# Kernel tuning notes

Hardware: AMD Instinct MI355X
Metric: run time of the kernel (lower is better)

Reference implementation:

```python
import jax, jax.numpy as jnp
import numpy as np

N, C, E = 50000, 128, 600000


def setup_inputs() -> dict:
    key = jax.random.key(0)
    ks = jax.random.split(key, 10)
    s = 1.0 / np.sqrt(C)
    x = jax.random.normal(ks[0], (N, C), jnp.float32)
    edge_index = jax.random.randint(ks[1], (2, E), 0, N)
    edge_weight = jax.random.uniform(ks[2], (E,), jnp.float32)
    # learned params
    p_score = jax.random.normal(ks[3], (C,), jnp.float32) * s      # TopKPooling projection
    W0 = jax.random.normal(ks[4], (C, C), jnp.float32) * s         # initial GCN weight
    w_ih = jax.random.normal(ks[5], (3 * C, C), jnp.float32) * s   # GRU input weights (r,z,n)
    w_hh = jax.random.normal(ks[6], (3 * C, C), jnp.float32) * s   # GRU hidden weights
    b_ih = jnp.zeros((3 * C,), jnp.float32)
    b_hh = jnp.zeros((3 * C,), jnp.float32)
    w_lin = jax.random.normal(ks[7], (1, C), jnp.float32) * s      # head Linear(C,1)
    b_lin = jnp.zeros((1,), jnp.float32)
    return dict(x=x, edge_index=edge_index, edge_weight=edge_weight,
                p_score=p_score, W0=W0, w_ih=w_ih, w_hh=w_hh,
                b_ih=b_ih, b_hh=b_hh, w_lin=w_lin, b_lin=b_lin)


def _evolve_gcnh(x, edge_index, edge_weight, p_score, W0, w_ih, w_hh, b_ih, b_hh):
    n, c = x.shape
    # --- TopKPooling: score = tanh((x.p)/||p||), keep top k=C nodes, scale by score
    score = jnp.tanh((x @ p_score) / jnp.linalg.norm(p_score))
    vals, perm = jax.lax.top_k(score, c)           # tanh monotone -> same perm as raw score
    x_tilde = x[perm] * vals[:, None]              # [C, C]
    # --- GRU single step: batch = C rows of the weight matrix, hidden = W0
    gi = x_tilde @ w_ih.T + b_ih                   # [C, 3C]
    gh = W0 @ w_hh.T + b_hh                        # [C, 3C]
    i_r, i_z, i_n = jnp.split(gi, 3, axis=1)
    h_r, h_z, h_n = jnp.split(gh, 3, axis=1)
    r = jax.nn.sigmoid(i_r + h_r)
    z = jax.nn.sigmoid(i_z + h_z)
    ng = jnp.tanh(i_n + r * h_n)
    W = (1.0 - z) * ng + z * W0                    # evolved GCN weight [C, C]
    # --- GCNConv with fixed W: gcn_norm with self loops, then scatter-sum
    loops = jnp.arange(n)
    row = jnp.concatenate([edge_index[0], loops])  # source
    col = jnp.concatenate([edge_index[1], loops])  # target
    w = jnp.concatenate([edge_weight, jnp.ones((n,), edge_weight.dtype)])
    deg = jax.ops.segment_sum(w, col, num_segments=n)
    dis = jnp.where(deg > 0, jax.lax.rsqrt(jnp.where(deg > 0, deg, 1.0)), 0.0)
    norm = dis[row] * w * dis[col]                 # [E+N]
    xw = x @ W                                     # [N, C]
    out = jax.ops.segment_sum(norm[:, None] * xw[row], col, num_segments=n)
    return out


def reference(x, edge_index, edge_weight, p_score, W0, w_ih, w_hh, b_ih, b_hh, w_lin, b_lin):
    h = _evolve_gcnh(x, edge_index, edge_weight, p_score, W0, w_ih, w_hh, b_ih, b_hh)
    h = jax.nn.relu(h)
    return h @ w_lin.T + b_lin                     # [N, 1]
```

## Files before the change

kernel.cpp:

```cpp
#include <hip/hip_runtime.h>
#include <stdint.h>

#define C 128
#define RSTRIDE 64

typedef __attribute__((ext_vector_type(8))) short short8;
typedef __attribute__((ext_vector_type(4))) float f32x4;

__device__ __forceinline__ unsigned f32_orderable(float f) {
  unsigned u = __float_as_uint(f);
  return (u & 0x80000000u) ? ~u : (u | 0x80000000u);
}
__device__ __forceinline__ unsigned short f32_to_bf16_rn(float f) {
  unsigned u = __float_as_uint(f);
  unsigned rounding = 0x7FFFu + ((u >> 16) & 1u);
  return (unsigned short)((u + rounding) >> 16);
}
__device__ __forceinline__ float bf16_to_f32(unsigned short h) {
  return __uint_as_float(((unsigned)h) << 16);
}

__global__ __launch_bounds__(256) void k_score(const float* __restrict__ x,
                                               const float* __restrict__ p,
                                               float* __restrict__ score,
                                               unsigned* __restrict__ hist, int N) {
  int l = threadIdx.x & 63;
  int n = blockIdx.x * 4 + (threadIdx.x >> 6);
  if (n >= N) return;
  float2 xv = ((const float2*)(x + (size_t)n * C))[l];
  float2 pv = ((const float2*)p)[l];
  float s = xv.x * pv.x + xv.y * pv.y;
  for (int o = 32; o > 0; o >>= 1) s += __shfl_down(s, o, 64);
  if (l == 0) {
    score[n] = s;
    atomicAdd(&hist[f32_orderable(s) >> 16], 1u);
  }
}

__global__ void k_thresh(const unsigned* __restrict__ hist, unsigned* __restrict__ misc_u) {
  __shared__ unsigned csum[1024];
  __shared__ int tcs;
  int t = threadIdx.x;
  unsigned s = 0;
  const unsigned* hb = hist + t * 64;
  for (int b = 0; b < 64; ++b) s += hb[b];
  csum[t] = s;
  __syncthreads();
  for (int off = 1; off < 1024; off <<= 1) {
    unsigned v = (t + off < 1024) ? csum[t + off] : 0u;
    __syncthreads();
    csum[t] += v;
    __syncthreads();
  }
  unsigned St  = csum[t];
  unsigned St1 = (t < 1023) ? csum[t + 1] : 0u;
  if (St >= 128u && St1 < 128u) tcs = t;
  __syncthreads();
  if (t == 0) {
    int tc = tcs;
    unsigned cum = (tc < 1023) ? csum[tc + 1] : 0u;
    unsigned T = (unsigned)(tc * 64);
    for (int b = tc * 64 + 63; b >= tc * 64; --b) {
      cum += hist[b];
      if (cum >= 128u) { T = (unsigned)b; break; }
    }
    misc_u[1] = T;
  }
}

__global__ __launch_bounds__(256) void k_collect(const float* __restrict__ score,
                                                 unsigned* __restrict__ misc_u,
                                                 uint64_t* __restrict__ cand, int N) {
  int n = blockIdx.x * 256 + threadIdx.x;
  if (n >= N) return;
  unsigned T = misc_u[1];
  unsigned u = f32_orderable(score[n]);
  if ((u >> 16) >= T) {
    unsigned pos = atomicAdd(&misc_u[0], 1u);
    if (pos < 1024u) cand[pos] = ((uint64_t)u << 32) | (unsigned)(~n);
  }
}

__global__ void k_select(const unsigned* __restrict__ misc_u,
                         const float* __restrict__ p,
                         const uint64_t* __restrict__ cand,
                         int* __restrict__ perm, float* __restrict__ vals) {
  __shared__ uint64_t keys[1024];
  __shared__ float s_inv;
  int t = threadIdx.x;
  if (t < 64) {
    float2 v = ((const float2*)p)[t];
    float s = v.x * v.x + v.y * v.y;
    for (int o = 32; o > 0; o >>= 1) s += __shfl_down(s, o, 64);
    if (t == 0) s_inv = 1.0f / sqrtf(s);
  }
  unsigned M = misc_u[0];
  if (M > 1024u) M = 1024u;
  keys[t] = (t < (int)M) ? cand[t] : 0ull;
  __syncthreads();
  for (int size = 2; size <= 1024; size <<= 1) {
    for (int stride = size >> 1; stride > 0; stride >>= 1) {
      int pr = t ^ stride;
      if (pr > t) {
        uint64_t a = keys[t], b = keys[pr];
        bool desc = ((t & size) == 0);
        if (desc ? (a < b) : (a > b)) { keys[t] = b; keys[pr] = a; }
      }
      __syncthreads();
    }
  }
  if (t < C) {
    uint64_t key = keys[t];
    unsigned n = ~(unsigned)(key & 0xFFFFFFFFull);
    unsigned u = (unsigned)(key >> 32);
    unsigned bbits = (u & 0x80000000u) ? (u & 0x7FFFFFFFu) : ~u;
    float s = __uint_as_float(bbits);
    perm[t] = (int)n;
    vals[t] = tanhf(s * s_inv);
  }
}

__global__ __launch_bounds__(128) void k_gru(const float* __restrict__ x,
                                             const int* __restrict__ perm,
                                             const float* __restrict__ vals,
                                             const float* __restrict__ W0,
                                             const float* __restrict__ w_ih,
                                             const float* __restrict__ w_hh,
                                             const float* __restrict__ b_ih,
                                             const float* __restrict__ b_hh,
                                             float* __restrict__ W) {
  __shared__ float xt[C], h0[C];
  int i = blockIdx.x, j = threadIdx.x;
  xt[j] = x[(size_t)perm[i] * C + j] * vals[i];
  h0[j] = W0[i * C + j];
  __syncthreads();
  float ir = b_ih[j], iz = b_ih[C + j], in_ = b_ih[2 * C + j];
  float hr = b_hh[j], hz = b_hh[C + j], hn  = b_hh[2 * C + j];
  const float4* wr = (const float4*)(w_ih + (size_t)j * C);
  const float4* wz = (const float4*)(w_ih + (size_t)(C + j) * C);
  const float4* wn = (const float4*)(w_ih + (size_t)(2 * C + j) * C);
  const float4* vr = (const float4*)(w_hh + (size_t)j * C);
  const float4* vz = (const float4*)(w_hh + (size_t)(C + j) * C);
  const float4* vn = (const float4*)(w_hh + (size_t)(2 * C + j) * C);
  const float4* xt4 = (const float4*)xt;
  const float4* h04 = (const float4*)h0;
  for (int k = 0; k < C / 4; ++k) {
    float4 xv = xt4[k], hv = h04[k], a;
    a = wr[k]; ir  += xv.x * a.x + xv.y * a.y + xv.z * a.z + xv.w * a.w;
    a = wz[k]; iz  += xv.x * a.x + xv.y * a.y + xv.z * a.z + xv.w * a.w;
    a = wn[k]; in_ += xv.x * a.x + xv.y * a.y + xv.z * a.z + xv.w * a.w;
    a = vr[k]; hr  += hv.x * a.x + hv.y * a.y + hv.z * a.z + hv.w * a.w;
    a = vz[k]; hz  += hv.x * a.x + hv.y * a.y + hv.z * a.z + hv.w * a.w;
    a = vn[k]; hn  += hv.x * a.x + hv.y * a.y + hv.z * a.z + hv.w * a.w;
  }
  float r  = 1.0f / (1.0f + expf(-(ir + hr)));
  float z  = 1.0f / (1.0f + expf(-(iz + hz)));
  float ng = tanhf(in_ + r * hn);
  W[i * C + j] = (1.0f - z) * ng + z * h0[j];
}

__global__ __launch_bounds__(256) void k_wsplit(const float* __restrict__ W,
                                                unsigned short* __restrict__ Bhi,
                                                unsigned short* __restrict__ Blo) {
  int gtid = blockIdx.x * 256 + threadIdx.x;
  int tile = gtid >> 6;
  int l = gtid & 63;
  int ct = tile >> 2, kt = tile & 3;
  int j = ct * 16 + (l & 15);
  int kbase = kt * 32 + (l >> 4) * 8;
  size_t o = (size_t)(tile * 64 + l) * 8;
#pragma unroll
  for (int e = 0; e < 8; ++e) {
    float w = W[(size_t)(kbase + e) * C + j];
    unsigned short hi = f32_to_bf16_rn(w);
    float rem = w - bf16_to_f32(hi);
    Bhi[o + e] = hi;
    Blo[o + e] = f32_to_bf16_rn(rem);
  }
}

__global__ __launch_bounds__(256) void k_xw(const float* __restrict__ x,
                                            const unsigned short* __restrict__ Bhi,
                                            const unsigned short* __restrict__ Blo,
                                            unsigned short* __restrict__ xwh, int N) {
  int wid = threadIdx.x >> 6;
  int l = threadIdx.x & 63;
  int rt = blockIdx.x * 4 + wid;
  int r0 = rt * 16;
  if (r0 >= N) return;
  int row16 = l & 15;
  int kgrp = l >> 4;

  short8 ahi[4], alo[4];
#pragma unroll
  for (int kt = 0; kt < 4; ++kt) {
    int r = r0 + row16;
    if (r >= N) r = N - 1;
    const float* xp = x + (size_t)r * C + kt * 32 + kgrp * 8;
    float4 a0 = *(const float4*)xp;
    float4 a1 = *(const float4*)(xp + 4);
    float v[8] = {a0.x, a0.y, a0.z, a0.w, a1.x, a1.y, a1.z, a1.w};
#pragma unroll
    for (int e = 0; e < 8; ++e) {
      unsigned short hi = f32_to_bf16_rn(v[e]);
      float rem = v[e] - bf16_to_f32(hi);
      ahi[kt][e] = (short)hi;
      alo[kt][e] = (short)f32_to_bf16_rn(rem);
    }
  }

  f32x4 acc[8];
#pragma unroll
  for (int ct = 0; ct < 8; ++ct) acc[ct] = (f32x4){0.f, 0.f, 0.f, 0.f};

#pragma unroll
  for (int ct = 0; ct < 8; ++ct) {
#pragma unroll
    for (int kt = 0; kt < 4; ++kt) {
      const short8 bhi = *(const short8*)(Bhi + (size_t)((ct * 4 + kt) * 64 + l) * 8);
      const short8 blo = *(const short8*)(Blo + (size_t)((ct * 4 + kt) * 64 + l) * 8);
      acc[ct] = __builtin_amdgcn_mfma_f32_16x16x32_bf16(ahi[kt], bhi, acc[ct], 0, 0, 0);
      acc[ct] = __builtin_amdgcn_mfma_f32_16x16x32_bf16(alo[kt], bhi, acc[ct], 0, 0, 0);
      acc[ct] = __builtin_amdgcn_mfma_f32_16x16x32_bf16(ahi[kt], blo, acc[ct], 0, 0, 0);
      acc[ct] = __builtin_amdgcn_mfma_f32_16x16x32_bf16(alo[kt], blo, acc[ct], 0, 0, 0);
    }
  }

#pragma unroll
  for (int ct = 0; ct < 8; ++ct) {
    int col = ct * 16 + row16;
#pragma unroll
    for (int reg = 0; reg < 4; ++reg) {
      int row = r0 + kgrp * 4 + reg;
      if (row < N) xwh[(size_t)row * C + col] = f32_to_bf16_rn(acc[ct][reg]);
    }
  }
}

__global__ __launch_bounds__(256) void k_fill(const int* __restrict__ ei,
                                              const float* __restrict__ ew,
                                              int* __restrict__ cnt,
                                              unsigned* __restrict__ csr, int E) {
  int e = blockIdx.x * 256 + threadIdx.x;
  if (e >= E) return;
  int src = ei[e];
  int dst = ei[E + e];
  int r = atomicAdd(&cnt[dst], 1);
  if (r > RSTRIDE - 1) r = RSTRIDE - 1;
  unsigned ent = ((unsigned)f32_to_bf16_rn(ew[e]) << 16) | (unsigned)src;
  csr[((size_t)dst << 6) + r] = ent;
}

__global__ __launch_bounds__(256) void k_rowdeg(const unsigned* __restrict__ csr,
                                                const int* __restrict__ cnt,
                                                float* __restrict__ dis, int N) {
  int tid = threadIdx.x;
  int n = blockIdx.x * 32 + (tid >> 3);
  if (n >= N) return;
  int l = tid & 7;
  int c = cnt[n];
  if (c > RSTRIDE) c = RSTRIDE;
  const unsigned* row = csr + ((size_t)n << 6);
  float s = 0.0f;
  for (int i = l; i < c; i += 8) s += bf16_to_f32((unsigned short)(row[i] >> 16));
  for (int o = 4; o > 0; o >>= 1) s += __shfl_down(s, o, 8);
  if (l == 0) dis[n] = rsqrtf(1.0f + s);
}

__device__ __forceinline__ float4 bf16x4_to_f32(uint2 pk) {
  float4 r;
  r.x = __uint_as_float(pk.x << 16);
  r.y = __uint_as_float(pk.x & 0xFFFF0000u);
  r.z = __uint_as_float(pk.y << 16);
  r.w = __uint_as_float(pk.y & 0xFFFF0000u);
  return r;
}
__global__ __launch_bounds__(256) void k_gather_final(const unsigned* __restrict__ csr,
                                                      const int* __restrict__ cnt,
                                                      const unsigned short* __restrict__ xwh,
                                                      const float* __restrict__ dis,
                                                      const float* __restrict__ w_lin,
                                                      const float* __restrict__ b_lin,
                                                      float* __restrict__ out, int N) {
  int tid = threadIdx.x;
  int n = blockIdx.x * 8 + (tid >> 5);
  if (n >= N) return;
  int l = tid & 31;
  const unsigned* row = csr + ((size_t)n << 6);
  int c = cnt[n];
  if (c > RSTRIDE) c = RSTRIDE;
  float4 acc = make_float4(0.f, 0.f, 0.f, 0.f);
  int i = 0;
  for (; i + 7 < c; i += 8) {
    unsigned n0 = row[i],   n1 = row[i+1], n2 = row[i+2], n3 = row[i+3];
    unsigned n4 = row[i+4], n5 = row[i+5], n6 = row[i+6], n7 = row[i+7];
    int s0 = n0 & 0xFFFF, s1 = n1 & 0xFFFF, s2 = n2 & 0xFFFF, s3 = n3 & 0xFFFF;
    int s4 = n4 & 0xFFFF, s5 = n5 & 0xFFFF, s6 = n6 & 0xFFFF, s7 = n7 & 0xFFFF;
    float w0 = bf16_to_f32((unsigned short)(n0 >> 16)) * dis[s0];
    float w1 = bf16_to_f32((unsigned short)(n1 >> 16)) * dis[s1];
    float w2 = bf16_to_f32((unsigned short)(n2 >> 16)) * dis[s2];
    float w3 = bf16_to_f32((unsigned short)(n3 >> 16)) * dis[s3];
    float w4 = bf16_to_f32((unsigned short)(n4 >> 16)) * dis[s4];
    float w5 = bf16_to_f32((unsigned short)(n5 >> 16)) * dis[s5];
    float w6 = bf16_to_f32((unsigned short)(n6 >> 16)) * dis[s6];
    float w7 = bf16_to_f32((unsigned short)(n7 >> 16)) * dis[s7];
    uint2 p0 = ((const uint2*)(xwh + (size_t)s0 * C))[l];
    uint2 p1 = ((const uint2*)(xwh + (size_t)s1 * C))[l];
    uint2 p2 = ((const uint2*)(xwh + (size_t)s2 * C))[l];
    uint2 p3 = ((const uint2*)(xwh + (size_t)s3 * C))[l];
    uint2 p4 = ((const uint2*)(xwh + (size_t)s4 * C))[l];
    uint2 p5 = ((const uint2*)(xwh + (size_t)s5 * C))[l];
    uint2 p6 = ((const uint2*)(xwh + (size_t)s6 * C))[l];
    uint2 p7 = ((const uint2*)(xwh + (size_t)s7 * C))[l];
    float4 v0 = bf16x4_to_f32(p0), v1 = bf16x4_to_f32(p1);
    float4 v2 = bf16x4_to_f32(p2), v3 = bf16x4_to_f32(p3);
    float4 v4 = bf16x4_to_f32(p4), v5 = bf16x4_to_f32(p5);
    float4 v6 = bf16x4_to_f32(p6), v7 = bf16x4_to_f32(p7);
    acc.x += w0*v0.x + w1*v1.x + w2*v2.x + w3*v3.x + w4*v4.x + w5*v5.x + w6*v6.x + w7*v7.x;
    acc.y += w0*v0.y + w1*v1.y + w2*v2.y + w3*v3.y + w4*v4.y + w5*v5.y + w6*v6.y + w7*v7.y;
    acc.z += w0*v0.z + w1*v1.z + w2*v2.z + w3*v3.z + w4*v4.z + w5*v5.z + w6*v6.z + w7*v7.z;
    acc.w += w0*v0.w + w1*v1.w + w2*v2.w + w3*v3.w + w4*v4.w + w5*v5.w + w6*v6.w + w7*v7.w;
  }
  for (; i < c; ++i) {
    unsigned n0 = row[i];
    int s0 = n0 & 0xFFFF;
    float w0 = bf16_to_f32((unsigned short)(n0 >> 16)) * dis[s0];
    uint2 p0 = ((const uint2*)(xwh + (size_t)s0 * C))[l];
    float4 v0 = bf16x4_to_f32(p0);
    acc.x += w0 * v0.x;
    acc.y += w0 * v0.y;
    acc.z += w0 * v0.z;
    acc.w += w0 * v0.w;
  }
  float dn = dis[n];
  uint2 ps = ((const uint2*)(xwh + (size_t)n * C))[l];
  float4 xv = bf16x4_to_f32(ps);
  acc.x = fmaf(dn, xv.x, acc.x) * dn;
  acc.y = fmaf(dn, xv.y, acc.y) * dn;
  acc.z = fmaf(dn, xv.z, acc.z) * dn;
  acc.w = fmaf(dn, xv.w, acc.w) * dn;
  float4 wl = ((const float4*)w_lin)[l];
  float psum = fmaxf(acc.x, 0.f) * wl.x + fmaxf(acc.y, 0.f) * wl.y
             + fmaxf(acc.z, 0.f) * wl.z + fmaxf(acc.w, 0.f) * wl.w;
  for (int o = 16; o > 0; o >>= 1) psum += __shfl_down(psum, o, 32);
  if (l == 0) out[n] = psum + b_lin[0];
}

extern "C" void kernel_launch(void* const* d_in, const int* in_sizes, int n_in,
                              void* d_out, int out_size, void* d_ws, size_t ws_size,
                              hipStream_t stream) {
  const float* x     = (const float*)d_in[0];
  const int*   ei    = (const int*)d_in[1];
  const float* ew    = (const float*)d_in[2];
  const float* p     = (const float*)d_in[3];
  const float* W0    = (const float*)d_in[4];
  const float* w_ih  = (const float*)d_in[5];
  const float* w_hh  = (const float*)d_in[6];
  const float* b_ih  = (const float*)d_in[7];
  const float* b_hh  = (const float*)d_in[8];
  const float* w_lin = (const float*)d_in[9];
  const float* b_lin = (const float*)d_in[10];
  int N = in_sizes[0] / C;
  int E = in_sizes[2];
  int NB = (N + 255) / 256;

  char* ws = (char*)d_ws;
  size_t off = 0;
  auto alloc = [&](size_t bytes) -> void* {
    void* q = ws + off;
    off = (off + bytes + 255) & ~(size_t)255;
    return q;
  };
  unsigned short* xwh = (unsigned short*)alloc((size_t)N * C * 2);
  unsigned* csr    = (unsigned*)alloc((size_t)N * RSTRIDE * 4);
  float*    score  = (float*)alloc((size_t)N * 4);
  float*    dis    = (float*)alloc((size_t)N * 4);
  int*      cnt    = (int*)alloc((size_t)N * 4);
  unsigned* hist   = (unsigned*)alloc(65536 * 4);
  uint64_t* cand   = (uint64_t*)alloc(1024 * 8);
  unsigned* misc_u = (unsigned*)alloc(256);
  int*      perm   = (int*)alloc(C * 4);
  float*    vals   = (float*)alloc(C * 4);
  float*    W      = (float*)alloc(C * C * 4);
  unsigned short* Bhi = (unsigned short*)alloc(C * C * 2);
  unsigned short* Blo = (unsigned short*)alloc(C * C * 2);

  hipMemsetAsync(hist, 0, 65536 * 4, stream);
  hipMemsetAsync(misc_u, 0, 256, stream);
  hipMemsetAsync(cnt, 0, (size_t)N * 4, stream);

  k_score<<<(N + 3) / 4, 256, 0, stream>>>(x, p, score, hist, N);
  k_thresh<<<1, 1024, 0, stream>>>(hist, misc_u);
  k_collect<<<NB, 256, 0, stream>>>(score, misc_u, cand, N);
  k_select<<<1, 1024, 0, stream>>>(misc_u, p, cand, perm, vals);
  k_gru<<<C, C, 0, stream>>>(x, perm, vals, W0, w_ih, w_hh, b_ih, b_hh, W);
  k_wsplit<<<8, 256, 0, stream>>>(W, Bhi, Blo);
  {
    int rowtiles = (N + 15) / 16;
    int blocks = (rowtiles + 3) / 4;
    k_xw<<<blocks, 256, 0, stream>>>(x, Bhi, Blo, xwh, N);
  }
  k_fill<<<(E + 255) / 256, 256, 0, stream>>>(ei, ew, cnt, csr, E);
  k_rowdeg<<<(N + 31) / 32, 256, 0, stream>>>(csr, cnt, dis, N);
  k_gather_final<<<(N + 7) / 8, 256, 0, stream>>>(csr, cnt, xwh, dis,
                                                  w_lin, b_lin, (float*)d_out, N);
}
```

Baseline: 258.5 us.

## Fuse score/CSR fill and topk/rowdeg kernels, unroll gather edge loop

After: 259.5 us. About the same (+0.4%).

```diff
diff --git a/kernel.cpp b/kernel.cpp
--- a/kernel.cpp
+++ b/kernel.cpp
@@ -20,103 +20,132 @@
   return __uint_as_float(((unsigned)h) << 16);
 }
 
-__global__ __launch_bounds__(256) void k_score(const float* __restrict__ x,
-                                               const float* __restrict__ p,
-                                               float* __restrict__ score,
-                                               unsigned* __restrict__ hist, int N) {
-  int l = threadIdx.x & 63;
-  int n = blockIdx.x * 4 + (threadIdx.x >> 6);
-  if (n >= N) return;
-  float2 xv = ((const float2*)(x + (size_t)n * C))[l];
-  float2 pv = ((const float2*)p)[l];
-  float s = xv.x * pv.x + xv.y * pv.y;
-  for (int o = 32; o > 0; o >>= 1) s += __shfl_down(s, o, 64);
-  if (l == 0) {
-    score[n] = s;
-    atomicAdd(&hist[f32_orderable(s) >> 16], 1u);
-  }
-}
-
-__global__ void k_thresh(const unsigned* __restrict__ hist, unsigned* __restrict__ misc_u) {
-  __shared__ unsigned csum[1024];
-  __shared__ int tcs;
+__global__ __launch_bounds__(256) void k_score_fill(const float* __restrict__ x,
+                                                    const float* __restrict__ p,
+                                                    float* __restrict__ score,
+                                                    unsigned* __restrict__ hist, int N,
+                                                    const int* __restrict__ ei,
+                                                    const float* __restrict__ ew,
+                                                    int* __restrict__ cnt,
+                                                    unsigned* __restrict__ csr, int E,
+                                                    int SB) {
+  int b = blockIdx.x;
+  if (b < SB) {
+    int l = threadIdx.x & 63;
+    int n = b * 4 + (threadIdx.x >> 6);
+    if (n >= N) return;
+    float2 xv = ((const float2*)(x + (size_t)n * C))[l];
+    float2 pv = ((const float2*)p)[l];
+    float s = xv.x * pv.x + xv.y * pv.y;
+    for (int o = 32; o > 0; o >>= 1) s += __shfl_down(s, o, 64);
+    if (l == 0) {
+      score[n] = s;
+      atomicAdd(&hist[f32_orderable(s) >> 16], 1u);
+    }
+  } else {
+    int e = (b - SB) * 256 + threadIdx.x;
+    if (e >= E) return;
+    int src = ei[e];
+    int dst = ei[E + e];
+    int r = atomicAdd(&cnt[dst], 1);
+    if (r > RSTRIDE - 1) r = RSTRIDE - 1;
+    unsigned ent = ((unsigned)f32_to_bf16_rn(ew[e]) << 16) | (unsigned)src;
+    csr[((size_t)dst << 6) + r] = ent;
+  }
+}
+
+__global__ __launch_bounds__(1024) void k_topk_rowdeg(const unsigned* __restrict__ hist,
+                                                      const float* __restrict__ score,
+                                                      const float* __restrict__ p,
+                                                      int* __restrict__ perm,
+                                                      float* __restrict__ vals, int N,
+                                                      const unsigned* __restrict__ csr,
+                                                      const int* __restrict__ cnt,
+                                                      float* __restrict__ dis) {
   int t = threadIdx.x;
-  unsigned s = 0;
-  const unsigned* hb = hist + t * 64;
-  for (int b = 0; b < 64; ++b) s += hb[b];
-  csum[t] = s;
-  __syncthreads();
-  for (int off = 1; off < 1024; off <<= 1) {
-    unsigned v = (t + off < 1024) ? csum[t + off] : 0u;
-    __syncthreads();
-    csum[t] += v;
-    __syncthreads();
-  }
-  unsigned St  = csum[t];
-  unsigned St1 = (t < 1023) ? csum[t + 1] : 0u;
-  if (St >= 128u && St1 < 128u) tcs = t;
-  __syncthreads();
-  if (t == 0) {
-    int tc = tcs;
-    unsigned cum = (tc < 1023) ? csum[tc + 1] : 0u;
-    unsigned T = (unsigned)(tc * 64);
-    for (int b = tc * 64 + 63; b >= tc * 64; --b) {
-      cum += hist[b];
-      if (cum >= 128u) { T = (unsigned)b; break; }
-    }
-    misc_u[1] = T;
-  }
-}
-
-__global__ __launch_bounds__(256) void k_collect(const float* __restrict__ score,
-                                                 unsigned* __restrict__ misc_u,
-                                                 uint64_t* __restrict__ cand, int N) {
-  int n = blockIdx.x * 256 + threadIdx.x;
-  if (n >= N) return;
-  unsigned T = misc_u[1];
-  unsigned u = f32_orderable(score[n]);
-  if ((u >> 16) >= T) {
-    unsigned pos = atomicAdd(&misc_u[0], 1u);
-    if (pos < 1024u) cand[pos] = ((uint64_t)u << 32) | (unsigned)(~n);
-  }
-}
-
-__global__ void k_select(const unsigned* __restrict__ misc_u,
-                         const float* __restrict__ p,
-                         const uint64_t* __restrict__ cand,
-                         int* __restrict__ perm, float* __restrict__ vals) {
-  __shared__ uint64_t keys[1024];
-  __shared__ float s_inv;
-  int t = threadIdx.x;
-  if (t < 64) {
-    float2 v = ((const float2*)p)[t];
-    float s = v.x * v.x + v.y * v.y;
-    for (int o = 32; o > 0; o >>= 1) s += __shfl_down(s, o, 64);
-    if (t == 0) s_inv = 1.0f / sqrtf(s);
-  }
-  unsigned M = misc_u[0];
-  if (M > 1024u) M = 1024u;
-  keys[t] = (t < (int)M) ? cand[t] : 0ull;
-  __syncthreads();
-  for (int size = 2; size <= 1024; size <<= 1) {
-    for (int stride = size >> 1; stride > 0; stride >>= 1) {
-      int pr = t ^ stride;
-      if (pr > t) {
-        uint64_t a = keys[t], b = keys[pr];
-        bool desc = ((t & size) == 0);
-        if (desc ? (a < b) : (a > b)) { keys[t] = b; keys[pr] = a; }
+  if (blockIdx.x == 0) {
+    __shared__ unsigned csum[1024];
+    __shared__ uint64_t keys[1024];
+    __shared__ int tcs;
+    __shared__ unsigned Ts, cnt_sh;
+    __shared__ float s_inv;
+    if (t < 64) {
+      float2 v = ((const float2*)p)[t];
+      float s = v.x * v.x + v.y * v.y;
+      for (int o = 32; o > 0; o >>= 1) s += __shfl_down(s, o, 64);
+      if (t == 0) s_inv = 1.0f / sqrtf(s);
+    }
+    if (t == 0) cnt_sh = 0;
+    unsigned s = 0;
+    const unsigned* hb = hist + t * 64;
+    for (int b = 0; b < 64; ++b) s += hb[b];
+    csum[t] = s;
+    __syncthreads();
+    for (int off = 1; off < 1024; off <<= 1) {
+      unsigned v = (t + off < 1024) ? csum[t + off] : 0u;
+      __syncthreads();
+      csum[t] += v;
+      __syncthreads();
+    }
+    unsigned St  = csum[t];
+    unsigned St1 = (t < 1023) ? csum[t + 1] : 0u;
+    if (St >= 128u && St1 < 128u) tcs = t;
+    __syncthreads();
+    if (t == 0) {
+      int tc = tcs;
+      unsigned cum = (tc < 1023) ? csum[tc + 1] : 0u;
+      unsigned T = (unsigned)(tc * 64);
+      for (int b = tc * 64 + 63; b >= tc * 64; --b) {
+        cum += hist[b];
+        if (cum >= 128u) { T = (unsigned)b; break; }
       }
-      __syncthreads();
-    }
-  }
-  if (t < C) {
-    uint64_t key = keys[t];
-    unsigned n = ~(unsigned)(key & 0xFFFFFFFFull);
-    unsigned u = (unsigned)(key >> 32);
-    unsigned bbits = (u & 0x80000000u) ? (u & 0x7FFFFFFFu) : ~u;
-    float s = __uint_as_float(bbits);
-    perm[t] = (int)n;
-    vals[t] = tanhf(s * s_inv);
+      Ts = T;
+    }
+    __syncthreads();
+    unsigned T = Ts;
+    for (int k = t; k < N; k += 1024) {
+      unsigned u = f32_orderable(score[k]);
+      if ((u >> 16) >= T) {
+        unsigned pos = atomicAdd(&cnt_sh, 1u);
+        if (pos < 1024u) keys[pos] = ((uint64_t)u << 32) | (unsigned)(~k);
+      }
+    }
+    __syncthreads();
+    unsigned M = cnt_sh;
+    if (M > 1024u) M = 1024u;
+    if (t >= (int)M) keys[t] = 0ull;
+    __syncthreads();
+    for (int size = 2; size <= 1024; size <<= 1) {
+      for (int stride = size >> 1; stride > 0; stride >>= 1) {
+        int pr = t ^ stride;
+        if (pr > t) {
+          uint64_t a = keys[t], b = keys[pr];
+          bool desc = ((t & size) == 0);
+          if (desc ? (a < b) : (a > b)) { keys[t] = b; keys[pr] = a; }
+        }
+        __syncthreads();
+      }
+    }
+    if (t < C) {
+      uint64_t key = keys[t];
+      unsigned n = ~(unsigned)(key & 0xFFFFFFFFull);
+      unsigned u = (unsigned)(key >> 32);
+      unsigned bbits = (u & 0x80000000u) ? (u & 0x7FFFFFFFu) : ~u;
+      float sc = __uint_as_float(bbits);
+      perm[t] = (int)n;
+      vals[t] = tanhf(sc * s_inv);
+    }
+  } else {
+    int n = (blockIdx.x - 1) * 128 + (t >> 3);
+    if (n >= N) return;
+    int l = t & 7;
+    int c = cnt[n];
+    if (c > RSTRIDE) c = RSTRIDE;
+    const unsigned* row = csr + ((size_t)n << 6);
+    float s = 0.0f;
+    for (int i = l; i < c; i += 8) s += bf16_to_f32((unsigned short)(row[i] >> 16));
+    for (int o = 4; o > 0; o >>= 1) s += __shfl_down(s, o, 8);
+    if (l == 0) dis[n] = rsqrtf(1.0f + s);
   }
 }
 
@@ -237,36 +266,6 @@
   }
 }
 
-__global__ __launch_bounds__(256) void k_fill(const int* __restrict__ ei,
-                                              const float* __restrict__ ew,
-                                              int* __restrict__ cnt,
-                                              unsigned* __restrict__ csr, int E) {
-  int e = blockIdx.x * 256 + threadIdx.x;
-  if (e >= E) return;
-  int src = ei[e];
-  int dst = ei[E + e];
-  int r = atomicAdd(&cnt[dst], 1);
-  if (r > RSTRIDE - 1) r = RSTRIDE - 1;
-  unsigned ent = ((unsigned)f32_to_bf16_rn(ew[e]) << 16) | (unsigned)src;
-  csr[((size_t)dst << 6) + r] = ent;
-}
-
-__global__ __launch_bounds__(256) void k_rowdeg(const unsigned* __restrict__ csr,
-                                                const int* __restrict__ cnt,
-                                                float* __restrict__ dis, int N) {
-  int tid = threadIdx.x;
-  int n = blockIdx.x * 32 + (tid >> 3);
-  if (n >= N) return;
-  int l = tid & 7;
-  int c = cnt[n];
-  if (c > RSTRIDE) c = RSTRIDE;
-  const unsigned* row = csr + ((size_t)n << 6);
-  float s = 0.0f;
-  for (int i = l; i < c; i += 8) s += bf16_to_f32((unsigned short)(row[i] >> 16));
-  for (int o = 4; o > 0; o >>= 1) s += __shfl_down(s, o, 8);
-  if (l == 0) dis[n] = rsqrtf(1.0f + s);
-}
-
 __device__ __forceinline__ float4 bf16x4_to_f32(uint2 pk) {
   float4 r;
   r.x = __uint_as_float(pk.x << 16);
@@ -290,47 +289,31 @@
   int c = cnt[n];
   if (c > RSTRIDE) c = RSTRIDE;
   float4 acc = make_float4(0.f, 0.f, 0.f, 0.f);
-  int i = 0;
-  for (; i + 7 < c; i += 8) {
-    unsigned n0 = row[i],   n1 = row[i+1], n2 = row[i+2], n3 = row[i+3];
-    unsigned n4 = row[i+4], n5 = row[i+5], n6 = row[i+6], n7 = row[i+7];
-    int s0 = n0 & 0xFFFF, s1 = n1 & 0xFFFF, s2 = n2 & 0xFFFF, s3 = n3 & 0xFFFF;
-    int s4 = n4 & 0xFFFF, s5 = n5 & 0xFFFF, s6 = n6 & 0xFFFF, s7 = n7 & 0xFFFF;
-    float w0 = bf16_to_f32((unsigned short)(n0 >> 16)) * dis[s0];
-    float w1 = bf16_to_f32((unsigned short)(n1 >> 16)) * dis[s1];
-    float w2 = bf16_to_f32((unsigned short)(n2 >> 16)) * dis[s2];
-    float w3 = bf16_to_f32((unsigned short)(n3 >> 16)) * dis[s3];
-    float w4 = bf16_to_f32((unsigned short)(n4 >> 16)) * dis[s4];
-    float w5 = bf16_to_f32((unsigned short)(n5 >> 16)) * dis[s5];
-    float w6 = bf16_to_f32((unsigned short)(n6 >> 16)) * dis[s6];
-    float w7 = bf16_to_f32((unsigned short)(n7 >> 16)) * dis[s7];
-    uint2 p0 = ((const uint2*)(xwh + (size_t)s0 * C))[l];
-    uint2 p1 = ((const uint2*)(xwh + (size_t)s1 * C))[l];
-    uint2 p2 = ((const uint2*)(xwh + (size_t)s2 * C))[l];
-    uint2 p3 = ((const uint2*)(xwh + (size_t)s3 * C))[l];
-    uint2 p4 = ((const uint2*)(xwh + (size_t)s4 * C))[l];
-    uint2 p5 = ((const uint2*)(xwh + (size_t)s5 * C))[l];
-    uint2 p6 = ((const uint2*)(xwh + (size_t)s6 * C))[l];
-    uint2 p7 = ((const uint2*)(xwh + (size_t)s7 * C))[l];
-    float4 v0 = bf16x4_to_f32(p0), v1 = bf16x4_to_f32(p1);
-    float4 v2 = bf16x4_to_f32(p2), v3 = bf16x4_to_f32(p3);
-    float4 v4 = bf16x4_to_f32(p4), v5 = bf16x4_to_f32(p5);
-    float4 v6 = bf16x4_to_f32(p6), v7 = bf16x4_to_f32(p7);
-    acc.x += w0*v0.x + w1*v1.x + w2*v2.x + w3*v3.x + w4*v4.x + w5*v5.x + w6*v6.x + w7*v7.x;
-    acc.y += w0*v0.y + w1*v1.y + w2*v2.y + w3*v3.y + w4*v4.y + w5*v5.y + w6*v6.y + w7*v7.y;
-    acc.z += w0*v0.z + w1*v1.z + w2*v2.z + w3*v3.z + w4*v4.z + w5*v5.z + w6*v6.z + w7*v7.z;
-    acc.w += w0*v0.w + w1*v1.w + w2*v2.w + w3*v3.w + w4*v4.w + w5*v5.w + w6*v6.w + w7*v7.w;
-  }
-  for (; i < c; ++i) {
-    unsigned n0 = row[i];
-    int s0 = n0 & 0xFFFF;
-    float w0 = bf16_to_f32((unsigned short)(n0 >> 16)) * dis[s0];
-    uint2 p0 = ((const uint2*)(xwh + (size_t)s0 * C))[l];
-    float4 v0 = bf16x4_to_f32(p0);
-    acc.x += w0 * v0.x;
-    acc.y += w0 * v0.y;
-    acc.z += w0 * v0.z;
-    acc.w += w0 * v0.w;
+
+  unsigned ent[16];
+#pragma unroll
+  for (int i = 0; i < 16; ++i) ent[i] = row[i];
+#pragma unroll
+  for (int i = 0; i < 16; ++i) {
+    int si = ent[i] & 0xFFFF;
+    float wi = (i < c) ? bf16_to_f32((unsigned short)(ent[i] >> 16)) * dis[si] : 0.0f;
+    uint2 pk = ((const uint2*)(xwh + (size_t)si * C))[l];
+    float4 v = bf16x4_to_f32(pk);
+    acc.x += wi * v.x;
+    acc.y += wi * v.y;
+    acc.z += wi * v.z;
+    acc.w += wi * v.w;
+  }
+  for (int i = 16; i < c; ++i) {
+    unsigned e0 = row[i];
+    int s0 = e0 & 0xFFFF;
+    float w0 = bf16_to_f32((unsigned short)(e0 >> 16)) * dis[s0];
+    uint2 pk = ((const uint2*)(xwh + (size_t)s0 * C))[l];
+    float4 v = bf16x4_to_f32(pk);
+    acc.x += w0 * v.x;
+    acc.y += w0 * v.y;
+    acc.z += w0 * v.z;
+    acc.w += w0 * v.w;
   }
   float dn = dis[n];
   uint2 ps = ((const uint2*)(xwh + (size_t)n * C))[l];
@@ -362,7 +345,6 @@
   const float* b_lin = (const float*)d_in[10];
   int N = in_sizes[0] / C;
   int E = in_sizes[2];
-  int NB = (N + 255) / 256;
 
   char* ws = (char*)d_ws;
   size_t off = 0;
@@ -375,24 +357,23 @@
   unsigned* csr    = (unsigned*)alloc((size_t)N * RSTRIDE * 4);
   float*    score  = (float*)alloc((size_t)N * 4);
   float*    dis    = (float*)alloc((size_t)N * 4);
+  size_t zstart = off;
+  unsigned* hist   = (unsigned*)alloc(65536 * 4);
   int*      cnt    = (int*)alloc((size_t)N * 4);
-  unsigned* hist   = (unsigned*)alloc(65536 * 4);
-  uint64_t* cand   = (uint64_t*)alloc(1024 * 8);
-  unsigned* misc_u = (unsigned*)alloc(256);
+  size_t zend = off;
   int*      perm   = (int*)alloc(C * 4);
   float*    vals   = (float*)alloc(C * 4);
   float*    W      = (float*)alloc(C * C * 4);
   unsigned short* Bhi = (unsigned short*)alloc(C * C * 2);
   unsigned short* Blo = (unsigned short*)alloc(C * C * 2);
 
-  hipMemsetAsync(hist, 0, 65536 * 4, stream);
-  hipMemsetAsync(misc_u, 0, 256, stream);
-  hipMemsetAsync(cnt, 0, (size_t)N * 4, stream);
-
-  k_score<<<(N + 3) / 4, 256, 0, stream>>>(x, p, score, hist, N);
-  k_thresh<<<1, 1024, 0, stream>>>(hist, misc_u);
-  k_collect<<<NB, 256, 0, stream>>>(score, misc_u, cand, N);
-  k_select<<<1, 1024, 0, stream>>>(misc_u, p, cand, perm, vals);
+  hipMemsetAsync(ws + zstart, 0, zend - zstart, stream);
+
+  int SB = (N + 3) / 4;
+  int FB = (E + 255) / 256;
+  k_score_fill<<<SB + FB, 256, 0, stream>>>(x, p, score, hist, N, ei, ew, cnt, csr, E, SB);
+  int RB = (N + 127) / 128;
+  k_topk_rowdeg<<<1 + RB, 1024, 0, stream>>>(hist, score, p, perm, vals, N, csr, cnt, dis);
   k_gru<<<C, C, 0, stream>>>(x, perm, vals, W0, w_ih, w_hh, b_ih, b_hh, W);
   k_wsplit<<<8, 256, 0, stream>>>(W, Bhi, Blo);
   {
@@ -400,8 +381,6 @@
     int blocks = (rowtiles + 3) / 4;
     k_xw<<<blocks, 256, 0, stream>>>(x, Bhi, Blo, xwh, N);
   }
-  k_fill<<<(E + 255) / 256, 256, 0, stream>>>(ei, ew, cnt, csr, E);
-  k_rowdeg<<<(N + 31) / 32, 256, 0, stream>>>(csr, cnt, dis, N);
   k_gather_final<<<(N + 7) / 8, 256, 0, stream>>>(csr, cnt, xwh, dis,
                                                   w_lin, b_lin, (float*)d_out, N);
 }
```

## Fuse top-k selection stages with row-degree pass and fold W split into GRU

Applied to the files above, without the earlier changes.

New measurement: 267.8 us. +3.6%, slower.

```diff
diff --git a/kernel.cpp b/kernel.cpp
--- a/kernel.cpp
+++ b/kernel.cpp
@@ -18,6 +18,14 @@
 }
 __device__ __forceinline__ float bf16_to_f32(unsigned short h) {
   return __uint_as_float(((unsigned)h) << 16);
+}
+__device__ __forceinline__ float4 bf16x4_to_f32(uint2 pk) {
+  float4 r;
+  r.x = __uint_as_float(pk.x << 16);
+  r.y = __uint_as_float(pk.x & 0xFFFF0000u);
+  r.z = __uint_as_float(pk.y << 16);
+  r.w = __uint_as_float(pk.y & 0xFFFF0000u);
+  return r;
 }
 
 __global__ __launch_bounds__(256) void k_score(const float* __restrict__ x,
@@ -37,86 +45,111 @@
   }
 }
 
-__global__ void k_thresh(const unsigned* __restrict__ hist, unsigned* __restrict__ misc_u) {
-  __shared__ unsigned csum[1024];
-  __shared__ int tcs;
+__global__ __launch_bounds__(256) void k_fill(const int* __restrict__ ei,
+                                              const float* __restrict__ ew,
+                                              int* __restrict__ cnt,
+                                              unsigned* __restrict__ csr, int E) {
+  int e = blockIdx.x * 256 + threadIdx.x;
+  if (e >= E) return;
+  int src = ei[e];
+  int dst = ei[E + e];
+  int r = atomicAdd(&cnt[dst], 1);
+  if (r > RSTRIDE - 1) r = RSTRIDE - 1;
+  unsigned ent = ((unsigned)f32_to_bf16_rn(ew[e]) << 16) | (unsigned)src;
+  csr[((size_t)dst << 6) + r] = ent;
+}
+
+__global__ __launch_bounds__(1024) void k_topk_rowdeg(const unsigned* __restrict__ hist,
+                                                      const float* __restrict__ score,
+                                                      const float* __restrict__ p,
+                                                      int* __restrict__ perm,
+                                                      float* __restrict__ vals, int N,
+                                                      const unsigned* __restrict__ csr,
+                                                      const int* __restrict__ cnt,
+                                                      float* __restrict__ dis) {
   int t = threadIdx.x;
-  unsigned s = 0;
-  const unsigned* hb = hist + t * 64;
-  for (int b = 0; b < 64; ++b) s += hb[b];
-  csum[t] = s;
-  __syncthreads();
-  for (int off = 1; off < 1024; off <<= 1) {
-    unsigned v = (t + off < 1024) ? csum[t + off] : 0u;
-    __syncthreads();
-    csum[t] += v;
-    __syncthreads();
-  }
-  unsigned St  = csum[t];
-  unsigned St1 = (t < 1023) ? csum[t + 1] : 0u;
-  if (St >= 128u && St1 < 128u) tcs = t;
-  __syncthreads();
-  if (t == 0) {
-    int tc = tcs;
-    unsigned cum = (tc < 1023) ? csum[tc + 1] : 0u;
-    unsigned T = (unsigned)(tc * 64);
-    for (int b = tc * 64 + 63; b >= tc * 64; --b) {
-      cum += hist[b];
-      if (cum >= 128u) { T = (unsigned)b; break; }
-    }
-    misc_u[1] = T;
-  }
-}
-
-__global__ __launch_bounds__(256) void k_collect(const float* __restrict__ score,
-                                                 unsigned* __restrict__ misc_u,
-                                                 uint64_t* __restrict__ cand, int N) {
-  int n = blockIdx.x * 256 + threadIdx.x;
-  if (n >= N) return;
-  unsigned T = misc_u[1];
-  unsigned u = f32_orderable(score[n]);
-  if ((u >> 16) >= T) {
-    unsigned pos = atomicAdd(&misc_u[0], 1u);
-    if (pos < 1024u) cand[pos] = ((uint64_t)u << 32) | (unsigned)(~n);
-  }
-}
-
-__global__ void k_select(const unsigned* __restrict__ misc_u,
-                         const float* __restrict__ p,
-                         const uint64_t* __restrict__ cand,
-                         int* __restrict__ perm, float* __restrict__ vals) {
-  __shared__ uint64_t keys[1024];
-  __shared__ float s_inv;
-  int t = threadIdx.x;
-  if (t < 64) {
-    float2 v = ((const float2*)p)[t];
-    float s = v.x * v.x + v.y * v.y;
-    for (int o = 32; o > 0; o >>= 1) s += __shfl_down(s, o, 64);
-    if (t == 0) s_inv = 1.0f / sqrtf(s);
-  }
-  unsigned M = misc_u[0];
-  if (M > 1024u) M = 1024u;
-  keys[t] = (t < (int)M) ? cand[t] : 0ull;
-  __syncthreads();
-  for (int size = 2; size <= 1024; size <<= 1) {
-    for (int stride = size >> 1; stride > 0; stride >>= 1) {
-      int pr = t ^ stride;
-      if (pr > t) {
-        uint64_t a = keys[t], b = keys[pr];
-        bool desc = ((t & size) == 0);
-        if (desc ? (a < b) : (a > b)) { keys[t] = b; keys[pr] = a; }
+  if (blockIdx.x == 0) {
+    __shared__ unsigned csum[1024];
+    __shared__ uint64_t keys[1024];
+    __shared__ int tcs;
+    __shared__ unsigned Ts, cnt_sh;
+    __shared__ float s_inv;
+    if (t < 64) {
+      float2 v = ((const float2*)p)[t];
+      float s = v.x * v.x + v.y * v.y;
+      for (int o = 32; o > 0; o >>= 1) s += __shfl_down(s, o, 64);
+      if (t == 0) s_inv = 1.0f / sqrtf(s);
+    }
+    if (t == 0) cnt_sh = 0;
+    unsigned s = 0;
+    const unsigned* hb = hist + t * 64;
+    for (int b = 0; b < 64; ++b) s += hb[b];
+    csum[t] = s;
+    __syncthreads();
+    for (int off = 1; off < 1024; off <<= 1) {
+      unsigned v = (t + off < 1024) ? csum[t + off] : 0u;
+      __syncthreads();
+      csum[t] += v;
+      __syncthreads();
+    }
+    unsigned St  = csum[t];
+    unsigned St1 = (t < 1023) ? csum[t + 1] : 0u;
+    if (St >= 128u && St1 < 128u) tcs = t;
+    __syncthreads();
+    if (t == 0) {
+      int tc = tcs;
+      unsigned cum = (tc < 1023) ? csum[tc + 1] : 0u;
+      unsigned T = (unsigned)(tc * 64);
+      for (int b = tc * 64 + 63; b >= tc * 64; --b) {
+        cum += hist[b];
+        if (cum >= 128u) { T = (unsigned)b; break; }
       }
-      __syncthreads();
-    }
-  }
-  if (t < C) {
-    uint64_t key = keys[t];
-    unsigned n = ~(unsigned)(key & 0xFFFFFFFFull);
-    unsigned u = (unsigned)(key >> 32);
-    unsigned bbits = (u & 0x80000000u) ? (u & 0x7FFFFFFFu) : ~u;
-    float s = __uint_as_float(bbits);
-    perm[t] = (int)n;
-    vals[t] = tanhf(s * s_inv);
+      Ts = T;
+    }
+    __syncthreads();
+    unsigned T = Ts;
+    for (int k = t; k < N; k += 1024) {
+      unsigned u = f32_orderable(score[k]);
+      if ((u >> 16) >= T) {
+        unsigned pos = atomicAdd(&cnt_sh, 1u);
+        if (pos < 1024u) keys[pos] = ((uint64_t)u << 32) | (unsigned)(~k);
+      }
+    }
+    __syncthreads();
+    unsigned M = cnt_sh;
+    if (M > 1024u) M = 1024u;
+    if (t >= (int)M) keys[t] = 0ull;
+    __syncthreads();
+    for (int size = 2; size <= 1024; size <<= 1) {
+      for (int stride = size >> 1; stride > 0; stride >>= 1) {
+        int pr = t ^ stride;
+        if (pr > t) {
+          uint64_t a = keys[t], b = keys[pr];
+          bool desc = ((t & size) == 0);
+          if (desc ? (a < b) : (a > b)) { keys[t] = b; keys[pr] = a; }
+        }
+        __syncthreads();
+      }
+    }
+    if (t < C) {
+      uint64_t key = keys[t];
+      unsigned n = ~(unsigned)(key & 0xFFFFFFFFull);
+      unsigned u = (unsigned)(key >> 32);
+      unsigned bbits = (u & 0x80000000u) ? (u & 0x7FFFFFFFu) : ~u;
+      perm[t] = (int)n;
+      vals[t] = tanhf(__uint_as_float(bbits) * s_inv);
+    }
+  } else {
+    int n = (blockIdx.x - 1) * 128 + (t >> 3);
+    if (n >= N) return;
+    int l = t & 7;
+    int c = cnt[n];
+    if (c > RSTRIDE) c = RSTRIDE;
+    const unsigned* row = csr + ((size_t)n << 6);
+    float s = 0.0f;
+    for (int i = l; i < c; i += 8) s += bf16_to_f32((unsigned short)(row[i] >> 16));
+    for (int o = 4; o > 0; o >>= 1) s += __shfl_down(s, o, 8);
+    if (l == 0) dis[n] = rsqrtf(1.0f + s);
   }
 }
 
@@ -128,7 +161,8 @@
                                              const float* __restrict__ w_hh,
                                              const float* __restrict__ b_ih,
                                              const float* __restrict__ b_hh,
-                                             float* __restrict__ W) {
+                                             unsigned short* __restrict__ Bhi,
+                                             unsigned short* __restrict__ Blo) {
   __shared__ float xt[C], h0[C];
   int i = blockIdx.x, j = threadIdx.x;
   xt[j] = x[(size_t)perm[i] * C + j] * vals[i];
@@ -156,27 +190,15 @@
   float r  = 1.0f / (1.0f + expf(-(ir + hr)));
   float z  = 1.0f / (1.0f + expf(-(iz + hz)));
   float ng = tanhf(in_ + r * hn);
-  W[i * C + j] = (1.0f - z) * ng + z * h0[j];
-}
-
-__global__ __launch_bounds__(256) void k_wsplit(const float* __restrict__ W,
-                                                unsigned short* __restrict__ Bhi,
-                                                unsigned short* __restrict__ Blo) {
-  int gtid = blockIdx.x * 256 + threadIdx.x;
-  int tile = gtid >> 6;
-  int l = gtid & 63;
-  int ct = tile >> 2, kt = tile & 3;
-  int j = ct * 16 + (l & 15);
-  int kbase = kt * 32 + (l >> 4) * 8;
-  size_t o = (size_t)(tile * 64 + l) * 8;
-#pragma unroll
-  for (int e = 0; e < 8; ++e) {
-    float w = W[(size_t)(kbase + e) * C + j];
-    unsigned short hi = f32_to_bf16_rn(w);
-    float rem = w - bf16_to_f32(hi);
-    Bhi[o + e] = hi;
-    Blo[o + e] = f32_to_bf16_rn(rem);
-  }
+  float w = (1.0f - z) * ng + z * h0[j];
+  int tile = (j >> 4) * 4 + (i >> 5);
+  int l2 = (j & 15) | (((i >> 3) & 3) << 4);
+  int e2 = i & 7;
+  size_t o = ((size_t)(tile * 64 + l2)) * 8 + e2;
+  unsigned short hi = f32_to_bf16_rn(w);
+  float rem = w - bf16_to_f32(hi);
+  Bhi[o] = hi;
+  Blo[o] = f32_to_bf16_rn(rem);
 }
 
 __global__ __launch_bounds__(256) void k_xw(const float* __restrict__ x,
@@ -237,44 +259,6 @@
   }
 }
 
-__global__ __launch_bounds__(256) void k_fill(const int* __restrict__ ei,
-                                              const float* __restrict__ ew,
-                                              int* __restrict__ cnt,
-                                              unsigned* __restrict__ csr, int E) {
-  int e = blockIdx.x * 256 + threadIdx.x;
-  if (e >= E) return;
-  int src = ei[e];
-  int dst = ei[E + e];
-  int r = atomicAdd(&cnt[dst], 1);
-  if (r > RSTRIDE - 1) r = RSTRIDE - 1;
-  unsigned ent = ((unsigned)f32_to_bf16_rn(ew[e]) << 16) | (unsigned)src;
-  csr[((size_t)dst << 6) + r] = ent;
-}
-
-__global__ __launch_bounds__(256) void k_rowdeg(const unsigned* __restrict__ csr,
-                                                const int* __restrict__ cnt,
-                                                float* __restrict__ dis, int N) {
-  int tid = threadIdx.x;
-  int n = blockIdx.x * 32 + (tid >> 3);
-  if (n >= N) return;
-  int l = tid & 7;
-  int c = cnt[n];
-  if (c > RSTRIDE) c = RSTRIDE;
-  const unsigned* row = csr + ((size_t)n << 6);
-  float s = 0.0f;
-  for (int i = l; i < c; i += 8) s += bf16_to_f32((unsigned short)(row[i] >> 16));
-  for (int o = 4; o > 0; o >>= 1) s += __shfl_down(s, o, 8);
-  if (l == 0) dis[n] = rsqrtf(1.0f + s);
-}
-
-__device__ __forceinline__ float4 bf16x4_to_f32(uint2 pk) {
-  float4 r;
-  r.x = __uint_as_float(pk.x << 16);
-  r.y = __uint_as_float(pk.x & 0xFFFF0000u);
-  r.z = __uint_as_float(pk.y << 16);
-  r.w = __uint_as_float(pk.y & 0xFFFF0000u);
-  return r;
-}
 __global__ __launch_bounds__(256) void k_gather_final(const unsigned* __restrict__ csr,
                                                       const int* __restrict__ cnt,
                                                       const unsigned short* __restrict__ xwh,
@@ -362,7 +346,6 @@
   const float* b_lin = (const float*)d_in[10];
   int N = in_sizes[0] / C;
   int E = in_sizes[2];
-  int NB = (N + 255) / 256;
 
   char* ws = (char*)d_ws;
   size_t off = 0;
@@ -375,33 +358,26 @@
   unsigned* csr    = (unsigned*)alloc((size_t)N * RSTRIDE * 4);
   float*    score  = (float*)alloc((size_t)N * 4);
   float*    dis    = (float*)alloc((size_t)N * 4);
+  size_t zstart = off;
+  unsigned* hist   = (unsigned*)alloc(65536 * 4);
   int*      cnt    = (int*)alloc((size_t)N * 4);
-  unsigned* hist   = (unsigned*)alloc(65536 * 4);
-  uint64_t* cand   = (uint64_t*)alloc(1024 * 8);
-  unsigned* misc_u = (unsigned*)alloc(256);
+  size_t zend = off;
   int*      perm   = (int*)alloc(C * 4);
   float*    vals   = (float*)alloc(C * 4);
-  float*    W      = (float*)alloc(C * C * 4);
   unsigned short* Bhi = (unsigned short*)alloc(C * C * 2);
   unsigned short* Blo = (unsigned short*)alloc(C * C * 2);
 
-  hipMemsetAsync(hist, 0, 65536 * 4, stream);
-  hipMemsetAsync(misc_u, 0, 256, stream);
-  hipMemsetAsync(cnt, 0, (size_t)N * 4, stream);
+  hipMemsetAsync(ws + zstart, 0, zend - zstart, stream);
 
   k_score<<<(N + 3) / 4, 256, 0, stream>>>(x, p, score, hist, N);
-  k_thresh<<<1, 1024, 0, stream>>>(hist, misc_u);
-  k_collect<<<NB, 256, 0, stream>>>(score, misc_u, cand, N);
-  k_select<<<1, 1024, 0, stream>>>(misc_u, p, cand, perm, vals);
-  k_gru<<<C, C, 0, stream>>>(x, perm, vals, W0, w_ih, w_hh, b_ih, b_hh, W);
-  k_wsplit<<<8, 256, 0, stream>>>(W, Bhi, Blo);
+  k_fill<<<(E + 255) / 256, 256, 0, stream>>>(ei, ew, cnt, csr, E);
+  int RB = (N + 127) / 128;
+  k_topk_rowdeg<<<1 + RB, 1024, 0, stream>>>(hist, score, p, perm, vals, N, csr, cnt, dis);
+  k_gru<<<C, C, 0, stream>>>(x, perm, vals, W0, w_ih, w_hh, b_ih, b_hh, Bhi, Blo);
   {
     int rowtiles = (N + 15) / 16;
-    int blocks = (rowtiles + 3) / 4;
-    k_xw<<<blocks, 256, 0, stream>>>(x, Bhi, Blo, xwh, N);
-  }
-  k_fill<<<(E + 255) / 256, 256, 0, stream>>>(ei, ew, cnt, csr, E);
-  k_rowdeg<<<(N + 31) / 32, 256, 0, stream>>>(csr, cnt, dis, N);
+    k_xw<<<(rowtiles + 3) / 4, 256, 0, stream>>>(x, Bhi, Blo, xwh, N);
+  }
   k_gather_final<<<(N + 7) / 8, 256, 0, stream>>>(csr, cnt, xwh, dis,
                                                   w_lin, b_lin, (float*)d_out, N);
 }
```
